# Kernel tuning notes

Measured on AMD Instinct MI355X. Metric: run time of the kernel, lower is better.

Reference implementation:

```python
import jax, jax.numpy as jnp
import numpy as np

NUM_HEADS = 16
HEAD_DIM = 64
ROPE_BASE = 10000.0


def _rope_cos_sin(seq_len, head_dim, dtype):
    inv_freq = 1.0 / (ROPE_BASE ** (jnp.arange(0, head_dim, 2, dtype=jnp.float32) / head_dim))
    t = jnp.arange(seq_len, dtype=jnp.float32)
    freqs = t[:, None] * inv_freq[None, :]          # (S, head_dim/2)
    emb = jnp.concatenate([freqs, freqs], axis=-1)  # (S, head_dim)
    return jnp.cos(emb).astype(dtype), jnp.sin(emb).astype(dtype)


def _rotate_half(x):
    x1, x2 = jnp.split(x, 2, axis=-1)
    return jnp.concatenate([-x2, x1], axis=-1)


def setup_inputs() -> dict:
    key = jax.random.key(0)
    k1, k2, k3 = jax.random.split(key, 3)
    B, S, D = 2, 2048, 1024
    x = jax.random.normal(k1, (B, S, D), dtype=jnp.float32)
    Wq = jax.random.normal(k2, (D, D), dtype=jnp.float32) * (D ** -0.5)
    Wkv = jax.random.normal(k3, (2 * D, D), dtype=jnp.float32) * (D ** -0.5)
    mask = jnp.tril(jnp.ones((S, S), dtype=jnp.int32))  # causal mask
    return {"x": x, "Wq": Wq, "Wkv": Wkv, "mask": mask}


def reference(x, Wq, Wkv, mask):
    B, S, D = x.shape
    H, Hd = NUM_HEADS, HEAD_DIM

    # projections (torch Linear: x @ W.T)
    q = (x @ Wq.T).reshape(B, S, H, Hd).transpose(0, 2, 1, 3)           # (B,H,S,Hd)
    kv = (x @ Wkv.T).reshape(B, S, H, Hd, 2).transpose(0, 2, 1, 3, 4)   # (B,H,S,Hd,2)
    k = kv[..., 0]
    v = kv[..., 1]

    # RoPE
    cos, sin = _rope_cos_sin(S, Hd, x.dtype)  # (S,Hd) broadcast over (B,H)
    q = q * cos + _rotate_half(q) * sin
    k = k * cos + _rotate_half(k) * sin

    # attention with full score materialization (faithful to source)
    scale = 1.0 / jnp.sqrt(jnp.asarray(Hd, dtype=x.dtype))
    scores = jnp.einsum('bhqd,bhkd->bhqk', q, k) * scale                # (B,H,S,S)
    scores = jnp.where(mask == 0, -jnp.inf, scores)
    attn = jax.nn.softmax(scores, axis=-1)
    out = jnp.einsum('bhqk,bhkd->bhqd', attn, v)                        # (B,H,S,Hd)
    return out.transpose(0, 2, 1, 3).reshape(B, S, D)
```

## Files before the change

### kernel.cpp

```cpp
#include <hip/hip_runtime.h>
#include <hip/hip_bf16.h>
#include <math.h>


typedef short bfrag __attribute__((ext_vector_type(8)));
typedef float f32x4 __attribute__((ext_vector_type(4)));

__device__ __forceinline__ float bf2f(ushort u) {
    union { uint i; float f; } v; v.i = ((uint)u) << 16; return v.f;
}
__device__ __forceinline__ ushort f2bf(float f) {
    union { uint i; float f; } v; v.f = f;
    uint u = v.i;
    return (ushort)((u + 0x7fffu + ((u >> 16) & 1u)) >> 16);
}

#define MFMA16 __builtin_amdgcn_mfma_f32_16x16x32_bf16

__device__ __forceinline__ void gl_lds16(const ushort* g, ushort* l) {
    __builtin_amdgcn_global_load_lds(
        (const __attribute__((address_space(1))) void*)g,
        (__attribute__((address_space(3))) void*)l, 16, 0, 0);
}

__global__ __launch_bounds__(256)
void cvt_bf16(const float* __restrict__ x, const float* __restrict__ wq,
              const float* __restrict__ wkv, ushort* __restrict__ xb,
              ushort* __restrict__ wb)
{
    const size_t NX = 4096u * 1024u, NWQ = 1024u * 1024u;
    size_t i8 = ((size_t)blockIdx.x * 256 + threadIdx.x) * 8;
    const float* src;
    ushort* dst;
    if (i8 < NX) { src = x + i8; dst = xb + i8; }
    else {
        size_t j = i8 - NX;
        dst = wb + j;
        src = (j < NWQ) ? (wq + j) : (wkv + (j - NWQ));
    }
    float4 a = *(const float4*)(src);
    float4 c = *(const float4*)(src + 4);
    ushort u[8];
    u[0] = f2bf(a.x); u[1] = f2bf(a.y); u[2] = f2bf(a.z); u[3] = f2bf(a.w);
    u[4] = f2bf(c.x); u[5] = f2bf(c.y); u[6] = f2bf(c.z); u[7] = f2bf(c.w);
    *(uint4*)dst = *(uint4*)u;
}

__global__ __launch_bounds__(256)
void rope_table(float2* __restrict__ tab)
{
    int t  = blockIdx.x * 256 + threadIdx.x;
    int fi = t & 31, s = t >> 5;
    float invf = (float)exp((double)fi * -0.28782313662425574);
    float thf  = (float)s * invf;
    const double TWO_PI = 6.283185307179586476925287;
    double th = (double)thf;
    double kq = __builtin_rint(th * (1.0 / TWO_PI));
    float r = (float)(th - kq * TWO_PI);
    tab[t] = make_float2(cosf(r), sinf(r));
}

__global__ __launch_bounds__(256)
void gemm_qkv(const ushort* __restrict__ xb, const ushort* __restrict__ wb,
              const float2* __restrict__ tab, ushort* __restrict__ Qb,
              ushort* __restrict__ Kb, ushort* __restrict__ Vt)
{
    __shared__ ushort Ash[128][32];
    __shared__ ushort Bsh[128][32];

    const int tid  = threadIdx.x;
    const int lane = tid & 63, wv = tid >> 6;
    const int quad = lane >> 4, li = lane & 15;
    const int m0 = blockIdx.x * 128, n0 = blockIdx.y * 128;

    f32x4 acc[2][8];
#pragma unroll
    for (int mi = 0; mi < 2; mi++)
#pragma unroll
        for (int j = 0; j < 8; j++) acc[mi][j] = (f32x4){0.f, 0.f, 0.f, 0.f};

    const int rsub = lane >> 2, kofs = (lane & 3) * 8;
    const ushort* gA0 = xb + (size_t)(m0 + wv * 32 + rsub) * 1024 + kofs;
    const ushort* gA1 = gA0 + 16 * 1024;
    const ushort* gB0 = wb + (size_t)(n0 + wv * 32 + rsub) * 1024 + kofs;
    const ushort* gB1 = gB0 + 16 * 1024;

    for (int k0 = 0; k0 < 1024; k0 += 32) {
        __syncthreads();
        gl_lds16(gA0 + k0, &Ash[wv * 32][0]);
        gl_lds16(gA1 + k0, &Ash[wv * 32 + 16][0]);
        gl_lds16(gB0 + k0, &Bsh[wv * 32][0]);
        gl_lds16(gB1 + k0, &Bsh[wv * 32 + 16][0]);
        __syncthreads();

        bfrag af[2], bf[8];
#pragma unroll
        for (int mi = 0; mi < 2; mi++)
            af[mi] = *(const bfrag*)&Ash[wv * 32 + mi * 16 + li][quad * 8];
#pragma unroll
        for (int j = 0; j < 8; j++)
            bf[j] = *(const bfrag*)&Bsh[j * 16 + li][quad * 8];
#pragma unroll
        for (int mi = 0; mi < 2; mi++)
#pragma unroll
            for (int j = 0; j < 8; j++)
                acc[mi][j] = MFMA16(af[mi], bf[j], acc[mi][j], 0, 0, 0);
    }

    if (n0 < 1024) {
        const int hbase = n0 >> 6;
#pragma unroll
        for (int mi = 0; mi < 2; mi++)
#pragma unroll
            for (int r = 0; r < 4; r++) {
                int m = m0 + wv * 32 + mi * 16 + quad * 4 + r;
                int bb = m >> 11, s = m & 2047;
                float2 t0 = tab[s * 32 + li];
                float2 t1 = tab[s * 32 + li + 16];
#pragma unroll
                for (int j = 0; j < 8; j++) {
                    float v  = acc[mi][j][r];
                    float vp = acc[mi][j ^ 2][r];
                    float2 tt = (j & 1) ? t1 : t0;
                    float rh = (j & 2) ? vp : -vp;
                    int h = hbase + (j >> 2), hd = (j & 3) * 16 + li;
                    Qb[(size_t)((bb * 16 + h) * 2048 + s) * 64 + hd] =
                        f2bf(v * tt.x + rh * tt.y);
                }
            }
    } else {
        const int h = (n0 - 1024) >> 7;
        const int li2 = li >> 1;
        if ((li & 1) == 0) {
#pragma unroll
            for (int mi = 0; mi < 2; mi++)
#pragma unroll
                for (int r = 0; r < 4; r++) {
                    int m = m0 + wv * 32 + mi * 16 + quad * 4 + r;
                    int bb = m >> 11, s = m & 2047;
                    float2 tt4[4];
#pragma unroll
                    for (int jj = 0; jj < 4; jj++)
                        tt4[jj] = tab[s * 32 + jj * 8 + li2];
#pragma unroll
                    for (int j = 0; j < 8; j++) {
                        float v  = acc[mi][j][r];
                        float vp = acc[mi][j ^ 4][r];
                        float2 tt = tt4[j & 3];
                        float rh = (j & 4) ? vp : -vp;
                        int hd = j * 8 + li2;
                        Kb[(size_t)((bb * 16 + h) * 2048 + s) * 64 + hd] =
                            f2bf(v * tt.x + rh * tt.y);
                    }
                }
        } else {
#pragma unroll
            for (int mi = 0; mi < 2; mi++) {
                int m4 = m0 + wv * 32 + mi * 16 + quad * 4;
                int bb = m4 >> 11, s0 = m4 & 2047;
#pragma unroll
                for (int j = 0; j < 8; j++) {
                    int hd = j * 8 + li2;
                    ushort u4[4];
#pragma unroll
                    for (int r = 0; r < 4; r++) u4[r] = f2bf(acc[mi][j][r]);
                    *(ushort4*)&Vt[(size_t)((bb * 16 + h) * 64 + hd) * 2048 + s0] =
                        *(ushort4*)u4;
                }
            }
        }
    }
}

__global__ __launch_bounds__(256)
void attn(const ushort* __restrict__ Qb, const ushort* __restrict__ Kb,
          const ushort* __restrict__ Vt, float* __restrict__ out)
{
    __shared__ ushort Ksh[64][72];
    __shared__ ushort Vsh[64][72];
    __shared__ ushort Psh[4][16][72];

    const int tid  = threadIdx.x;
    const int lane = tid & 63, w = tid >> 6;
    const int quad = lane >> 4, li = lane & 15;
    const int qt = ((31 - (int)blockIdx.x) + (int)blockIdx.y) & 31;
    const int bh = blockIdx.y;
    const int b = bh >> 4, h = bh & 15;

    const int qrow = qt * 64 + w * 16 + li;
    const ushort* qp = Qb + (size_t)(bh * 2048 + qrow) * 64;
    bfrag qa0 = *(const bfrag*)(qp + quad * 8);
    bfrag qa1 = *(const bfrag*)(qp + quad * 8 + 32);

    f32x4 o[4];
#pragma unroll
    for (int j = 0; j < 4; j++) o[j] = (f32x4){0.f, 0.f, 0.f, 0.f};
    float lrow[4] = {0.f, 0.f, 0.f, 0.f};

    const int srow = tid >> 2, sc0 = (tid & 3) * 16;
    const ushort* kbase = Kb + (size_t)bh * 2048 * 64;
    const ushort* vbase = Vt + (size_t)bh * 64 * 2048;
    const int qg0 = qt * 64 + w * 16 + quad * 4;

    uint4 ka, kb_, va, vb_;
    {
        const ushort* gk = kbase + (size_t)srow * 64 + sc0;
        ka  = *(const uint4*)gk;
        kb_ = *(const uint4*)(gk + 8);
        const ushort* gv = vbase + (size_t)srow * 2048 + sc0;
        va  = *(const uint4*)gv;
        vb_ = *(const uint4*)(gv + 8);
    }

    const float C = 0.125f * 1.4426950408889634f;

    for (int kt = 0; kt <= qt; ++kt) {
        __syncthreads();
        *(uint4*)&Ksh[srow][sc0]     = ka;
        *(uint4*)&Ksh[srow][sc0 + 8] = kb_;
        *(uint4*)&Vsh[srow][sc0]     = va;
        *(uint4*)&Vsh[srow][sc0 + 8] = vb_;
        __syncthreads();

        if (kt < qt) {
            const ushort* gk = kbase + (size_t)((kt + 1) * 64 + srow) * 64 + sc0;
            ka  = *(const uint4*)gk;
            kb_ = *(const uint4*)(gk + 8);
            const ushort* gv = vbase + (size_t)srow * 2048 + (kt + 1) * 64 + sc0;
            va  = *(const uint4*)gv;
            vb_ = *(const uint4*)(gv + 8);
        }

        f32x4 sc[4];
        __builtin_amdgcn_s_setprio(1);
#pragma unroll
        for (int j = 0; j < 4; j++) {
            bfrag kb0 = *(const bfrag*)&Ksh[j * 16 + li][quad * 8];
            bfrag kb1 = *(const bfrag*)&Ksh[j * 16 + li][quad * 8 + 32];
            f32x4 z = (f32x4){0.f, 0.f, 0.f, 0.f};
            z = MFMA16(qa0, kb0, z, 0, 0, 0);
            z = MFMA16(qa1, kb1, z, 0, 0, 0);
            sc[j] = z;
        }
        __builtin_amdgcn_s_setprio(0);

        if (kt == qt) {
#pragma unroll
            for (int j = 0; j < 4; j++) {
                int kg = kt * 64 + j * 16 + li;
#pragma unroll
                for (int r = 0; r < 4; r++)
                    sc[j][r] = (kg <= qg0 + r) ? sc[j][r] : -3.0e38f;
            }
        }

        float rsum[4] = {0.f, 0.f, 0.f, 0.f};
#pragma unroll
        for (int j = 0; j < 4; j++)
#pragma unroll
            for (int r = 0; r < 4; r++) {
                float pv = exp2f(sc[j][r] * C);
                uint pu = __float_as_uint(pv);
                Psh[w][quad * 4 + r][j * 16 + li] = (ushort)(pu >> 16);
                rsum[r] += __uint_as_float(pu & 0xffff0000u);
            }
#pragma unroll
        for (int off = 1; off < 16; off <<= 1)
#pragma unroll
            for (int r = 0; r < 4; r++)
                rsum[r] += __shfl_xor(rsum[r], off);
#pragma unroll
        for (int r = 0; r < 4; r++) lrow[r] += rsum[r];

        asm volatile("s_waitcnt lgkmcnt(0)" ::: "memory");
        bfrag pa0 = *(const bfrag*)&Psh[w][li][quad * 8];
        bfrag pa1 = *(const bfrag*)&Psh[w][li][quad * 8 + 32];

        __builtin_amdgcn_s_setprio(1);
#pragma unroll
        for (int j = 0; j < 4; j++) {
            bfrag vb0 = *(const bfrag*)&Vsh[j * 16 + li][quad * 8];
            bfrag vb1 = *(const bfrag*)&Vsh[j * 16 + li][quad * 8 + 32];
            o[j] = MFMA16(pa0, vb0, o[j], 0, 0, 0);
            o[j] = MFMA16(pa1, vb1, o[j], 0, 0, 0);
        }
        __builtin_amdgcn_s_setprio(0);
    }

#pragma unroll
    for (int j = 0; j < 4; j++)
#pragma unroll
        for (int r = 0; r < 4; r++) {
            int s = qt * 64 + w * 16 + quad * 4 + r;
            out[(size_t)(b * 2048 + s) * 1024 + h * 64 + j * 16 + li] =
                o[j][r] / lrow[r];
        }
}

extern "C" void kernel_launch(void* const* d_in, const int* in_sizes, int n_in,
                              void* d_out, int out_size, void* d_ws, size_t ws_size,
                              hipStream_t stream)
{
    (void)in_sizes; (void)n_in; (void)out_size; (void)ws_size;
    const float* x   = (const float*)d_in[0];
    const float* wq  = (const float*)d_in[1];
    const float* wkv = (const float*)d_in[2];

    ushort* xb = (ushort*)d_ws;
    ushort* wb = xb + (size_t)4096 * 1024;
    float2* tab = (float2*)(wb + (size_t)3072 * 1024);
    ushort* Qb = (ushort*)(tab + 65536);
    ushort* Kb = Qb + (size_t)2 * 16 * 2048 * 64;
    ushort* Vt = Kb + (size_t)2 * 16 * 2048 * 64;
    float* out = (float*)d_out;

    cvt_bf16<<<3584, 256, 0, stream>>>(x, wq, wkv, xb, wb);
    rope_table<<<256, 256, 0, stream>>>(tab);
    dim3 g1(32, 24);
    gemm_qkv<<<g1, 256, 0, stream>>>(xb, wb, tab, Qb, Kb, Vt);
    dim3 g4(32, 32);
    attn<<<g4, 256, 0, stream>>>(Qb, Kb, Vt, out);
}
```

Measured before the change: 201.2 us.

## Pack four causal query tiles per attention block and widen GEMM K-tile with swizzle

The attention kernel now gives each block four query tiles (t, 15-t, 16+t, 31-t) so every block does balanced causal work, and each K/V tile loaded into shared memory is reused across four query tiles. Scores are computed transposed (K as A operand), P is stored per tile, and row sums are finished at the end with shuffles. The grid drops to 256 blocks with launch_bounds(256,1). The QKV GEMM moves to a 64-wide K step with an XOR-swizzled LDS layout to cut bank conflicts and halve barrier count. Risks are higher register pressure and lower occupancy, since only 256 blocks now run.

```diff
diff --git a/kernel.cpp b/kernel.cpp
--- a/kernel.cpp
+++ b/kernel.cpp
@@ -13,6 +13,11 @@
     union { uint i; float f; } v; v.f = f;
     uint u = v.i;
     return (ushort)((u + 0x7fffu + ((u >> 16) & 1u)) >> 16);
+}
+__device__ __forceinline__ ushort f2bf_hw(float f) {
+    union { __hip_bfloat16 b; ushort u; } cv;
+    cv.b = __float2bfloat16(f);
+    return cv.u;
 }
 
 #define MFMA16 __builtin_amdgcn_mfma_f32_16x16x32_bf16
@@ -65,8 +70,8 @@
               const float2* __restrict__ tab, ushort* __restrict__ Qb,
               ushort* __restrict__ Kb, ushort* __restrict__ Vt)
 {
-    __shared__ ushort Ash[128][32];
-    __shared__ ushort Bsh[128][32];
+    __shared__ ushort Ash[128][64];
+    __shared__ ushort Bsh[128][64];
 
     const int tid  = threadIdx.x;
     const int lane = tid & 63, wv = tid >> 6;
@@ -79,32 +84,38 @@
 #pragma unroll
         for (int j = 0; j < 8; j++) acc[mi][j] = (f32x4){0.f, 0.f, 0.f, 0.f};
 
-    const int rsub = lane >> 2, kofs = (lane & 3) * 8;
-    const ushort* gA0 = xb + (size_t)(m0 + wv * 32 + rsub) * 1024 + kofs;
-    const ushort* gA1 = gA0 + 16 * 1024;
-    const ushort* gB0 = wb + (size_t)(n0 + wv * 32 + rsub) * 1024 + kofs;
-    const ushort* gB1 = gB0 + 16 * 1024;
-
-    for (int k0 = 0; k0 < 1024; k0 += 32) {
+    const int r8  = lane >> 3;
+    const int gch = ((lane & 7) ^ r8) * 8;
+    const ushort* gA = xb + (size_t)(m0 + wv * 32 + r8) * 1024 + gch;
+    const ushort* gB = wb + (size_t)(n0 + wv * 32 + r8) * 1024 + gch;
+
+    for (int k0 = 0; k0 < 1024; k0 += 64) {
         __syncthreads();
-        gl_lds16(gA0 + k0, &Ash[wv * 32][0]);
-        gl_lds16(gA1 + k0, &Ash[wv * 32 + 16][0]);
-        gl_lds16(gB0 + k0, &Bsh[wv * 32][0]);
-        gl_lds16(gB1 + k0, &Bsh[wv * 32 + 16][0]);
+#pragma unroll
+        for (int c = 0; c < 4; c++) {
+            gl_lds16(gA + (size_t)(c * 8) * 1024 + k0, &Ash[wv * 32 + c * 8][0]);
+            gl_lds16(gB + (size_t)(c * 8) * 1024 + k0, &Bsh[wv * 32 + c * 8][0]);
+        }
         __syncthreads();
 
-        bfrag af[2], bf[8];
-#pragma unroll
-        for (int mi = 0; mi < 2; mi++)
-            af[mi] = *(const bfrag*)&Ash[wv * 32 + mi * 16 + li][quad * 8];
-#pragma unroll
-        for (int j = 0; j < 8; j++)
-            bf[j] = *(const bfrag*)&Bsh[j * 16 + li][quad * 8];
-#pragma unroll
-        for (int mi = 0; mi < 2; mi++)
+        const int sw = li & 7;
+#pragma unroll
+        for (int ks = 0; ks < 2; ks++) {
+            bfrag af[2], bf[8];
+#pragma unroll
+            for (int mi = 0; mi < 2; mi++)
+                af[mi] = *(const bfrag*)
+                    &Ash[wv * 32 + mi * 16 + li][(((ks << 2) | quad) ^ sw) * 8];
 #pragma unroll
             for (int j = 0; j < 8; j++)
-                acc[mi][j] = MFMA16(af[mi], bf[j], acc[mi][j], 0, 0, 0);
+                bf[j] = *(const bfrag*)
+                    &Bsh[j * 16 + li][(((ks << 2) | quad) ^ sw) * 8];
+#pragma unroll
+            for (int mi = 0; mi < 2; mi++)
+#pragma unroll
+                for (int j = 0; j < 8; j++)
+                    acc[mi][j] = MFMA16(af[mi], bf[j], acc[mi][j], 0, 0, 0);
+        }
     }
 
     if (n0 < 1024) {
@@ -172,35 +183,46 @@
     }
 }
 
-__global__ __launch_bounds__(256)
+__global__ __launch_bounds__(256, 1)
 void attn(const ushort* __restrict__ Qb, const ushort* __restrict__ Kb,
           const ushort* __restrict__ Vt, float* __restrict__ out)
 {
     __shared__ ushort Ksh[64][72];
     __shared__ ushort Vsh[64][72];
-    __shared__ ushort Psh[4][16][72];
+    __shared__ ushort Psh[4][4][16][72];
 
     const int tid  = threadIdx.x;
     const int lane = tid & 63, w = tid >> 6;
     const int quad = lane >> 4, li = lane & 15;
-    const int qt = ((31 - (int)blockIdx.x) + (int)blockIdx.y) & 31;
-    const int bh = blockIdx.y;
+
+    const int l  = (int)blockIdx.x;
+    const int bh = l & 31;
+    const int t  = l >> 5;
     const int b = bh >> 4, h = bh & 15;
 
-    const int qrow = qt * 64 + w * 16 + li;
-    const ushort* qp = Qb + (size_t)(bh * 2048 + qrow) * 64;
-    bfrag qa0 = *(const bfrag*)(qp + quad * 8);
-    bfrag qa1 = *(const bfrag*)(qp + quad * 8 + 32);
-
-    f32x4 o[4];
-#pragma unroll
-    for (int j = 0; j < 4; j++) o[j] = (f32x4){0.f, 0.f, 0.f, 0.f};
+    const int qts[4] = {t, 15 - t, 16 + t, 31 - t};
+    const int ktmax = 31 - t;
+
+    int rows[4];
+    bfrag qa[4][2];
+#pragma unroll
+    for (int s = 0; s < 4; s++) {
+        rows[s] = qts[s] * 64 + w * 16 + li;
+        const ushort* qp = Qb + (size_t)(bh * 2048 + rows[s]) * 64;
+        qa[s][0] = *(const bfrag*)(qp + quad * 8);
+        qa[s][1] = *(const bfrag*)(qp + quad * 8 + 32);
+    }
+
+    f32x4 o[4][4];
+#pragma unroll
+    for (int s = 0; s < 4; s++)
+#pragma unroll
+        for (int j = 0; j < 4; j++) o[s][j] = (f32x4){0.f, 0.f, 0.f, 0.f};
     float lrow[4] = {0.f, 0.f, 0.f, 0.f};
 
     const int srow = tid >> 2, sc0 = (tid & 3) * 16;
     const ushort* kbase = Kb + (size_t)bh * 2048 * 64;
     const ushort* vbase = Vt + (size_t)bh * 64 * 2048;
-    const int qg0 = qt * 64 + w * 16 + quad * 4;
 
     uint4 ka, kb_, va, vb_;
     {
@@ -214,7 +236,7 @@
 
     const float C = 0.125f * 1.4426950408889634f;
 
-    for (int kt = 0; kt <= qt; ++kt) {
+    for (int kt = 0; kt <= ktmax; ++kt) {
         __syncthreads();
         *(uint4*)&Ksh[srow][sc0]     = ka;
         *(uint4*)&Ksh[srow][sc0 + 8] = kb_;
@@ -222,7 +244,7 @@
         *(uint4*)&Vsh[srow][sc0 + 8] = vb_;
         __syncthreads();
 
-        if (kt < qt) {
+        if (kt < ktmax) {
             const ushort* gk = kbase + (size_t)((kt + 1) * 64 + srow) * 64 + sc0;
             ka  = *(const uint4*)gk;
             kb_ = *(const uint4*)(gk + 8);
@@ -231,70 +253,98 @@
             vb_ = *(const uint4*)(gv + 8);
         }
 
-        f32x4 sc[4];
-        __builtin_amdgcn_s_setprio(1);
+        float rs[4] = {0.f, 0.f, 0.f, 0.f};
+
 #pragma unroll
         for (int j = 0; j < 4; j++) {
-            bfrag kb0 = *(const bfrag*)&Ksh[j * 16 + li][quad * 8];
-            bfrag kb1 = *(const bfrag*)&Ksh[j * 16 + li][quad * 8 + 32];
-            f32x4 z = (f32x4){0.f, 0.f, 0.f, 0.f};
-            z = MFMA16(qa0, kb0, z, 0, 0, 0);
-            z = MFMA16(qa1, kb1, z, 0, 0, 0);
-            sc[j] = z;
-        }
-        __builtin_amdgcn_s_setprio(0);
-
-        if (kt == qt) {
-#pragma unroll
-            for (int j = 0; j < 4; j++) {
-                int kg = kt * 64 + j * 16 + li;
-#pragma unroll
-                for (int r = 0; r < 4; r++)
-                    sc[j][r] = (kg <= qg0 + r) ? sc[j][r] : -3.0e38f;
-            }
-        }
-
-        float rsum[4] = {0.f, 0.f, 0.f, 0.f};
+            bfrag kf0 = *(const bfrag*)&Ksh[j * 16 + li][quad * 8];
+            bfrag kf1 = *(const bfrag*)&Ksh[j * 16 + li][quad * 8 + 32];
+
+            f32x4 z[4];
+            __builtin_amdgcn_s_setprio(1);
+#pragma unroll
+            for (int s = 0; s < 4; s++) {
+                if (kt <= qts[s]) {
+                    f32x4 zz = (f32x4){0.f, 0.f, 0.f, 0.f};
+                    zz = MFMA16(kf0, qa[s][0], zz, 0, 0, 0);
+                    zz = MFMA16(kf1, qa[s][1], zz, 0, 0, 0);
+                    z[s] = zz;
+                }
+            }
+            __builtin_amdgcn_s_setprio(0);
+
+            const int kg0 = kt * 64 + j * 16 + quad * 4;
+#pragma unroll
+            for (int s = 0; s < 4; s++) {
+                if (kt <= qts[s]) {
+                    if (kt == qts[s]) {
+#pragma unroll
+                        for (int r = 0; r < 4; r++)
+                            z[s][r] = (kg0 + r <= rows[s]) ? z[s][r] : -3.0e38f;
+                    }
+                    ushort pk[4];
+#pragma unroll
+                    for (int r = 0; r < 4; r++) {
+                        float pv = exp2f(z[s][r] * C);
+                        rs[s] += pv;
+                        pk[r] = f2bf_hw(pv);
+                    }
+                    *(ushort4*)&Psh[w][s][li][j * 16 + quad * 4] = *(ushort4*)pk;
+                }
+            }
+        }
+
+#pragma unroll
+        for (int s = 0; s < 4; s++) {
+            if (kt <= qts[s]) {
+                float v = rs[s];
+                v += __shfl_xor(v, 16);
+                v += __shfl_xor(v, 32);
+                lrow[s] += v;
+            }
+        }
+
+        asm volatile("s_waitcnt lgkmcnt(0)" ::: "memory");
+        bfrag pa[4][2];
+#pragma unroll
+        for (int s = 0; s < 4; s++) {
+            if (kt <= qts[s]) {
+                pa[s][0] = *(const bfrag*)&Psh[w][s][li][quad * 8];
+                pa[s][1] = *(const bfrag*)&Psh[w][s][li][quad * 8 + 32];
+            }
+        }
+
+#pragma unroll
+        for (int j = 0; j < 4; j++) {
+            bfrag vf0 = *(const bfrag*)&Vsh[j * 16 + li][quad * 8];
+            bfrag vf1 = *(const bfrag*)&Vsh[j * 16 + li][quad * 8 + 32];
+            __builtin_amdgcn_s_setprio(1);
+#pragma unroll
+            for (int s = 0; s < 4; s++) {
+                if (kt <= qts[s]) {
+                    o[s][j] = MFMA16(pa[s][0], vf0, o[s][j], 0, 0, 0);
+                    o[s][j] = MFMA16(pa[s][1], vf1, o[s][j], 0, 0, 0);
+                }
+            }
+            __builtin_amdgcn_s_setprio(0);
+        }
+    }
+
+#pragma unroll
+    for (int s = 0; s < 4; s++) {
+        float lf[4];
+#pragma unroll
+        for (int r = 0; r < 4; r++)
+            lf[r] = __shfl(lrow[s], (lane & 48) + quad * 4 + r);
 #pragma unroll
         for (int j = 0; j < 4; j++)
 #pragma unroll
             for (int r = 0; r < 4; r++) {
-                float pv = exp2f(sc[j][r] * C);
-                uint pu = __float_as_uint(pv);
-                Psh[w][quad * 4 + r][j * 16 + li] = (ushort)(pu >> 16);
-                rsum[r] += __uint_as_float(pu & 0xffff0000u);
-            }
-#pragma unroll
-        for (int off = 1; off < 16; off <<= 1)
-#pragma unroll
-            for (int r = 0; r < 4; r++)
-                rsum[r] += __shfl_xor(rsum[r], off);
-#pragma unroll
-        for (int r = 0; r < 4; r++) lrow[r] += rsum[r];
-
-        asm volatile("s_waitcnt lgkmcnt(0)" ::: "memory");
-        bfrag pa0 = *(const bfrag*)&Psh[w][li][quad * 8];
-        bfrag pa1 = *(const bfrag*)&Psh[w][li][quad * 8 + 32];
-
-        __builtin_amdgcn_s_setprio(1);
-#pragma unroll
-        for (int j = 0; j < 4; j++) {
-            bfrag vb0 = *(const bfrag*)&Vsh[j * 16 + li][quad * 8];
-            bfrag vb1 = *(const bfrag*)&Vsh[j * 16 + li][quad * 8 + 32];
-            o[j] = MFMA16(pa0, vb0, o[j], 0, 0, 0);
-            o[j] = MFMA16(pa1, vb1, o[j], 0, 0, 0);
-        }
-        __builtin_amdgcn_s_setprio(0);
-    }
-
-#pragma unroll
-    for (int j = 0; j < 4; j++)
-#pragma unroll
-        for (int r = 0; r < 4; r++) {
-            int s = qt * 64 + w * 16 + quad * 4 + r;
-            out[(size_t)(b * 2048 + s) * 1024 + h * 64 + j * 16 + li] =
-                o[j][r] / lrow[r];
-        }
+                int sr = qts[s] * 64 + w * 16 + quad * 4 + r;
+                out[(size_t)(b * 2048 + sr) * 1024 + h * 64 + j * 16 + li] =
+                    o[s][j][r] / lf[r];
+            }
+    }
 }
 
 extern "C" void kernel_launch(void* const* d_in, const int* in_sizes, int n_in,
@@ -318,6 +368,5 @@
     rope_table<<<256, 256, 0, stream>>>(tab);
     dim3 g1(32, 24);
     gemm_qkv<<<g1, 256, 0, stream>>>(xb, wb, tab, Qb, Kb, Vt);
-    dim3 g4(32, 32);
-    attn<<<g4, 256, 0, stream>>>(Qb, Kb, Vt, out);
-}
+    attn<<<256, 256, 0, stream>>>(Qb, Kb, Vt, out);
+}
```

Result: slower. 212.8 us (+5.8%).
